# Optimization experiments

Hardware: AMD Instinct MI355X
Metric: run time of the kernel (lower is better)

## Reference

```python
import jax, jax.numpy as jnp
import numpy as np

B, HH, WW, C, HEADS = 2, 128, 128, 256, 8
D = C // HEADS


def setup_inputs() -> dict:
    key = jax.random.key(0)
    ks = jax.random.split(key, 24)
    def nrm(k, shape, s=0.02):
        return jax.random.normal(k, shape, jnp.float32) * s
    inp = {
        'x_2': jax.random.normal(ks[0], (B, HH, WW, C), jnp.float32),
        'x_4': jax.random.normal(ks[1], (B, HH, WW, C), jnp.float32),
        'x_8': jax.random.normal(ks[2], (B, HH, WW, C), jnp.float32),
        'y':   jax.random.normal(ks[3], (B, HH, WW, C), jnp.float32),
        'Wqm': nrm(ks[4], (C, C)), 'Wkm': nrm(ks[5], (C, C)), 'Wvm': nrm(ks[6], (C, C)),
        'Wk2': nrm(ks[7], (C, C)), 'Wv2': nrm(ks[8], (C, C)),
        'Wk4': nrm(ks[9], (C, C)), 'Wv4': nrm(ks[10], (C, C)),
        'Wk8': nrm(ks[11], (C, C)), 'Wv8': nrm(ks[12], (C, C)),
        'rescalem': jnp.ones((HEADS, 1, 1), jnp.float32),
        'rescale2': jnp.ones((HEADS, 1, 1), jnp.float32),
        'rescale4': jnp.ones((HEADS, 1, 1), jnp.float32),
        'rescale8': jnp.ones((HEADS, 1, 1), jnp.float32),
        'Wproj': nrm(ks[13], (C, C)), 'bproj': jnp.zeros((C,), jnp.float32),
        'Wpos1': nrm(ks[14], (C, 1, 3, 3)), 'Wpos2': nrm(ks[15], (C, 1, 3, 3)),
    }
    return inp


def _l2norm(x):
    # F.normalize(p=2, dim=-1): x / max(||x||_2, eps)
    return x / jnp.maximum(jnp.linalg.norm(x, axis=-1, keepdims=True), 1e-12)


def _heads_T(t):
    # (b, n, h*d) -> (b, h, d, n)  (split heads then transpose last two dims)
    b, n, _ = t.shape
    return t.reshape(b, n, HEADS, D).transpose(0, 2, 3, 1)


def _dwconv(x, w):
    # x: NCHW, w: (C,1,3,3) depthwise
    return jax.lax.conv_general_dilated(
        x, w, (1, 1), 'SAME',
        dimension_numbers=('NCHW', 'OIHW', 'NCHW'),
        feature_group_count=C)


def reference(x_2, x_4, x_8, y,
              Wqm, Wkm, Wvm, Wk2, Wv2, Wk4, Wv4, Wk8, Wv8,
              rescalem, rescale2, rescale4, rescale8,
              Wproj, bproj, Wpos1, Wpos2):
    b, h, w, c = y.shape
    n = h * w
    x2 = x_2.reshape(b, n, c)
    x4 = x_4.reshape(b, n, c)
    x8 = x_8.reshape(b, n, c)
    yf = y.reshape(b, n, c)

    q_inpm = yf @ Wqm.T
    v_inpm = yf @ Wvm.T
    qm = _l2norm(_heads_T(q_inpm))  # (b,heads,d,n), L2-normalized over n

    def branch(k_inp, v_inp, rescale):
        k = _l2norm(_heads_T(k_inp))   # (b,heads,d,n)
        v = _heads_T(v_inp)            # (b,heads,d,n)
        attn = jnp.einsum('bhdn,bhen->bhde', k, qm) * rescale  # (b,heads,d,d)
        attn = jax.nn.softmax(attn, axis=-1)
        return jnp.einsum('bhde,bhen->bhdn', attn, v)

    # NOTE: original code uses rescale4 for the x8 branch (faithful to source).
    xo = (branch(yf @ Wkm.T, v_inpm, rescalem)
          + branch(x2 @ Wk2.T, x2 @ Wv2.T, rescale2)
          + branch(x4 @ Wk4.T, x4 @ Wv4.T, rescale4)
          + branch(x8 @ Wk8.T, x8 @ Wv8.T, rescale4))

    # (b,heads,d,n) -> (b,n,heads*d)
    xo = xo.transpose(0, 3, 1, 2).reshape(b, n, HEADS * D)
    out_c = (xo @ Wproj.T + bproj).reshape(b, h, w, c)

    p = v_inpm.reshape(b, h, w, c).transpose(0, 3, 1, 2)  # NCHW
    p = _dwconv(p, Wpos1)
    p = jax.nn.gelu(p, approximate=False)
    p = _dwconv(p, Wpos2)
    out_p = p.transpose(0, 2, 3, 1)

    return out_c + out_p
```

## Files before the change

### kernel.cpp

```cpp
#include <hip/hip_runtime.h>
#include <hip/hip_bf16.h>
#include <math.h>

typedef short bf16x8 __attribute__((ext_vector_type(8)));
typedef float f32x4 __attribute__((ext_vector_type(4)));

#define MFMA16(a,b,c) __builtin_amdgcn_mfma_f32_16x16x32_bf16(a,b,c,0,0,0)

__device__ inline short f2bf(float f){
  union{ __hip_bfloat16 h; short s; } u;
  u.h = __float2bfloat16(f);
  return u.s;
}
__device__ inline float bf2f(short s){
  uint32_t u = ((uint32_t)(uint16_t)s) << 16;
  return __builtin_bit_cast(float, u);
}
__device__ inline void store8bf(short* dst, float4 a, float4 b){
  union{ short s[8]; int4 q; } u;
  u.s[0]=f2bf(a.x); u.s[1]=f2bf(a.y); u.s[2]=f2bf(a.z); u.s[3]=f2bf(a.w);
  u.s[4]=f2bf(b.x); u.s[5]=f2bf(b.y); u.s[6]=f2bf(b.z); u.s[7]=f2bf(b.w);
  *(int4*)dst = u.q;
}

__device__ inline void gld16(const void* g, void* l){
  __builtin_amdgcn_global_load_lds(
      (const __attribute__((address_space(1))) unsigned int*)g,
      (__attribute__((address_space(3))) unsigned int*)l, 16, 0, 0);
}

__global__ __launch_bounds__(256) void k_cvt(const float* __restrict__ src, short* __restrict__ dst, int n){
  int i = blockIdx.x*256 + threadIdx.x;
  if(i < n) dst[i] = f2bf(src[i]);
}

__global__ __launch_bounds__(256) void k_wvt(const float* __restrict__ wm, const float* __restrict__ w2,
                                             const float* __restrict__ w4, const float* __restrict__ w8,
                                             short* __restrict__ wvT){
  int t = blockIdx.x*256 + threadIdx.x;
  int br = t >> 16; int rem = t & 65535; int a = rem >> 8, j = rem & 255;
  const float* w = (br==0)? wm : (br==1)? w2 : (br==2)? w4 : w8;
  wvT[t] = f2bf(w[j*256 + a]);
}

__global__ __launch_bounds__(256) void k_wT(const float* __restrict__ w1, const float* __restrict__ w2,
                                            float* __restrict__ wT){
  int t = blockIdx.x*256 + threadIdx.x;
  if(t >= 4608) return;
  int cv = t / 2304; int rem = t % 2304; int tap = rem >> 8; int c = rem & 255;
  const float* w = cv ? w2 : w1;
  wT[t] = w[c*9 + tap];
}

__global__ __launch_bounds__(256) void k_pack(const float* __restrict__ x2, const float* __restrict__ x4,
                                              const float* __restrict__ x8, const float* __restrict__ y,
                                              short* __restrict__ xt){
  int sb = blockIdx.z; int s = sb >> 1, b = sb & 1;
  const float* src = ((s==0)? y : (s==1)? x2 : (s==2)? x4 : x8) + (size_t)b*16384*256;
  __shared__ short tile[64*264];
  int t = threadIdx.x, l = t & 63, w = t >> 6;
  int n0 = blockIdx.x*64;
  #pragma unroll
  for(int p=0;p<16;++p){
    int row = p*4 + w;
    float4 v = *(const float4*)(src + (size_t)(n0+row)*256 + 4*l);
    union{ short s4[4]; int2 q; } u;
    u.s4[0]=f2bf(v.x); u.s4[1]=f2bf(v.y); u.s4[2]=f2bf(v.z); u.s4[3]=f2bf(v.w);
    *(int2*)&tile[row*264 + 4*l] = u.q;
  }
  __syncthreads();
  int c = t;
  short* outb = xt + ((size_t)sb*512 + (n0>>5))*8192;
  #pragma unroll
  for(int ti=0; ti<2; ++ti){
    union{ short v[32]; int4 q4[4]; } rowv;
    #pragma unroll
    for(int j=0;j<32;++j) rowv.v[j] = tile[(ti*32+j)*264 + c];
    char* ob = (char*)(outb + (size_t)ti*8192 + c*32);
    #pragma unroll
    for(int hi=0;hi<4;++hi)
      *(int4*)(ob + ((hi ^ (c&3))<<4)) = rowv.q4[hi];
  }
}

__device__ inline bf16x8 tfrag(const short* base, int c, int hi){
  int byte = c*64 + ((hi ^ (c&3))<<4);
  return *(const bf16x8*)((const char*)base + byte);
}

__global__ __launch_bounds__(512,2) void k_cov(const short* __restrict__ xt, float* __restrict__ covF){
  int jb = blockIdx.x;
  int ck = blockIdx.y;
  int j = jb >> 1, b = jb & 1;
  int t = threadIdx.x, l = t & 63, w = t >> 6;
  int lr = l & 15, hi = l >> 4;
  __shared__ short lds2[2][16384];
  int su = (j < 4) ? 0 : (j - 3);
  int sv = (j == 0) ? 0 : ((j < 4) ? j : (j - 3));
  int sym = (su == sv);
  const short* Ug = xt + (size_t)(su*2+b)*512*8192;
  const short* Vg = xt + (size_t)(sv*2+b)*512*8192;
  int nt0 = ck*32;

  f32x4 acc[2][16];
  #pragma unroll
  for(int i=0;i<2;++i)
    #pragma unroll
    for(int n2=0;n2<16;++n2) acc[i][n2] = (f32x4){0.f,0.f,0.f,0.f};

  #define STAGE(bufi, kk) do{                                                   \
    const short* Ut_ = Ug + (size_t)(nt0+(kk))*8192;                            \
    short* dst_ = &lds2[bufi][0];                                               \
    if(sym){                                                                    \
      _Pragma("unroll")                                                         \
      for(int i_=0;i_<2;++i_){ int ch_ = w*2+i_;                                \
        gld16(Ut_ + ch_*512 + l*8, dst_ + ch_*512); }                           \
    } else {                                                                    \
      const short* Vt_ = Vg + (size_t)(nt0+(kk))*8192;                          \
      _Pragma("unroll")                                                         \
      for(int i_=0;i_<4;++i_){ int ch_ = w*4+i_;                                \
        const short* g_ = (ch_<16) ? (Ut_ + ch_*512 + l*8)                      \
                                   : (Vt_ + (ch_-16)*512 + l*8);                \
        gld16(g_, dst_ + ch_*512); }                                            \
    }                                                                           \
  }while(0)

  const int vofs = sym ? 0 : 8192;

  STAGE(0, 0);
  __syncthreads();
  for(int k=0;k<32;++k){
    int cur = k & 1;
    if(k < 31) STAGE(cur^1, k+1);
    const short* Ub = &lds2[cur][0];
    const short* Vb = Ub + vofs;
    bf16x8 a0 = tfrag(Ub, w*32 + lr, hi);
    bf16x8 a1 = tfrag(Ub, w*32 + 16 + lr, hi);
    #pragma unroll
    for(int nt=0;nt<16;++nt){
      bf16x8 bb = tfrag(Vb, nt*16 + lr, hi);
      acc[0][nt] = MFMA16(a0, bb, acc[0][nt]);
      acc[1][nt] = MFMA16(a1, bb, acc[1][nt]);
    }
    __syncthreads();
  }
  #undef STAGE

  float* cov = covF + (size_t)jb*65536;
  #pragma unroll
  for(int rt=0;rt<2;++rt)
    #pragma unroll
    for(int nt=0;nt<16;++nt)
      #pragma unroll
      for(int r=0;r<4;++r){
        int row = w*32 + rt*16 + 4*hi + r;
        int col = nt*16 + lr;
        atomicAdd(&cov[(size_t)row*256 + col], acc[rt][nt][r]);
      }
}

__device__ inline void mm_32x256(const short (*wA)[264], const short* __restrict__ covbf,
                                 short (*tmp)[264], int t){
  int l = t & 63, w = t >> 6;
  int mt = w >> 1, ntb = (w & 1)*8;
  f32x4 acc[8];
  #pragma unroll
  for(int i=0;i<8;++i) acc[i] = (f32x4){0.f,0.f,0.f,0.f};
  #pragma unroll
  for(int kk=0; kk<8; ++kk){
    bf16x8 a = *(const bf16x8*)&wA[16*mt + (l&15)][kk*32 + 8*(l>>4)];
    #pragma unroll
    for(int n=0; n<8; ++n){
      int j = (ntb+n)*16 + (l&15);
      bf16x8 bb = *(const bf16x8*)&covbf[(size_t)j*256 + kk*32 + 8*(l>>4)];
      acc[n] = MFMA16(a, bb, acc[n]);
    }
  }
  #pragma unroll
  for(int n=0;n<8;++n)
    #pragma unroll
    for(int r=0;r<4;++r)
      tmp[16*mt + 4*(l>>4) + r][(ntb+n)*16 + (l&15)] = f2bf(acc[n][r]);
}
__device__ inline void mm_32x32(const short (*A)[264], const short (*Bw)[264], float (*M)[33], int t){
  int l = t & 63, w = t >> 6;
  int mt = w >> 1, nt = w & 1;
  f32x4 acc = (f32x4){0.f,0.f,0.f,0.f};
  #pragma unroll
  for(int kk=0; kk<8; ++kk){
    bf16x8 a = *(const bf16x8*)&A[16*mt + (l&15)][kk*32 + 8*(l>>4)];
    bf16x8 b = *(const bf16x8*)&Bw[16*nt + (l&15)][kk*32 + 8*(l>>4)];
    acc = MFMA16(a, b, acc);
  }
  #pragma unroll
  for(int r=0;r<4;++r)
    M[16*mt + 4*(l>>4) + r][16*nt + (l&15)] = acc[r];
}

__global__ __launch_bounds__(256) void k_attn(
    const float* __restrict__ Wq, const float* __restrict__ Wkm, const float* __restrict__ Wk2,
    const float* __restrict__ Wk4, const float* __restrict__ Wk8,
    const float* __restrict__ rsm, const float* __restrict__ rs2, const float* __restrict__ rs4,
    const short* __restrict__ covB, float* __restrict__ Aout){
  int h = blockIdx.x, b = blockIdx.y, br = blockIdx.z;
  int t = threadIdx.x;
  __shared__ short wk[32][264], wq[32][264], tmp[32][264];
  __shared__ float Ml[32][33];
  __shared__ float nrm[64];
  const float* Wk = (br==0)? Wkm : (br==1)? Wk2 : (br==2)? Wk4 : Wk8;
  {
    int d = t >> 3, c0 = (t & 7)*32;
    const float* pk = Wk + (size_t)(h*32+d)*256 + c0;
    const float* pq = Wq + (size_t)(h*32+d)*256 + c0;
    #pragma unroll
    for(int i=0;i<32;i+=8){
      float4 a1 = *(const float4*)(pk+i), a2 = *(const float4*)(pk+i+4);
      store8bf(&wk[d][c0+i], a1, a2);
      float4 b1 = *(const float4*)(pq+i), b2 = *(const float4*)(pq+i+4);
      store8bf(&wq[d][c0+i], b1, b2);
    }
  }
  __syncthreads();
  const short* cxy = covB + (size_t)(br*2+b)*65536;
  const short* cxx = (br==0)? cxy : covB + (size_t)(8 + (br-1)*2 + b)*65536;
  const short* cyy = covB + (size_t)b*65536;
  mm_32x256(wk, cxx, tmp, t); __syncthreads();
  mm_32x32(tmp, wk, Ml, t);   __syncthreads();
  if(t < 32) nrm[t] = Ml[t][t];
  __syncthreads();
  mm_32x256(wq, cyy, tmp, t); __syncthreads();
  mm_32x32(tmp, wq, Ml, t);   __syncthreads();
  if(t < 32) nrm[32+t] = Ml[t][t];
  __syncthreads();
  mm_32x256(wk, cxy, tmp, t); __syncthreads();
  mm_32x32(tmp, wq, Ml, t);   __syncthreads();
  if(t < 32){
    int d = t;
    const float* rs = (br==0)? rsm : (br==1)? rs2 : rs4;
    float rsv = rs[h];
    float invk = 1.f / fmaxf(sqrtf(fmaxf(nrm[d], 0.f)), 1e-12f);
    float lg[32]; float mx = -1e30f;
    #pragma unroll
    for(int e=0;e<32;++e){
      float invq = 1.f / fmaxf(sqrtf(fmaxf(nrm[32+e], 0.f)), 1e-12f);
      float v = Ml[d][e] * invk * invq * rsv;
      lg[e] = v; mx = fmaxf(mx, v);
    }
    float sum = 0.f;
    #pragma unroll
    for(int e=0;e<32;++e){ lg[e] = expf(lg[e]-mx); sum += lg[e]; }
    float inv = 1.f/sum;
    float* Ao = Aout + ((size_t)((br*2+b)*8 + h))*1024 + d*32;
    #pragma unroll
    for(int e=0;e<32;++e) Ao[e] = lg[e]*inv;
  }
}

__global__ __launch_bounds__(256) void k_qfold(const float* __restrict__ Wproj, const float* __restrict__ Ain,
                                               const short* __restrict__ wvT, short* __restrict__ qf){
  int cg = blockIdx.x, b = blockIdx.y, br = blockIdx.z;
  int t = threadIdx.x;
  __shared__ float Al[8*1036];
  __shared__ short pl[32][264];
  const float* Ag = Ain + (size_t)((br*2+b)*8)*1024;
  for(int i=t; i<8192; i+=256){
    int hh = i >> 10, dd = (i >> 5) & 31, ee = i & 31;
    Al[hh*1036 + dd*32 + ee] = Ag[i];
  }
  __syncthreads();
  {
    int c = cg*32 + (t >> 3), h = t & 7;
    const float* wpr = Wproj + (size_t)c*256 + h*32;
    float wp[32];
    #pragma unroll
    for(int i=0;i<32;i+=4){
      float4 v = *(const float4*)(wpr+i);
      wp[i]=v.x; wp[i+1]=v.y; wp[i+2]=v.z; wp[i+3]=v.w;
    }
    float pv[32];
    #pragma unroll
    for(int e=0;e<32;++e) pv[e]=0.f;
    const float* Ah = Al + h*1036;
    #pragma unroll
    for(int d=0; d<32; ++d){
      float wpd = wp[d];
      #pragma unroll
      for(int e=0;e<32;e+=4){
        float4 av = *(const float4*)&Ah[d*32+e];
        pv[e]   += wpd*av.x; pv[e+1] += wpd*av.y;
        pv[e+2] += wpd*av.z; pv[e+3] += wpd*av.w;
      }
    }
    #pragma unroll
    for(int e=0;e<32;++e) pl[t>>3][h*32+e] = f2bf(pv[e]);
  }
  __syncthreads();
  {
    int l = t & 63, w = t >> 6, mt = w >> 1, ntb = (w & 1)*8;
    const short* wvt = wvT + (size_t)br*65536;
    f32x4 acc[8];
    #pragma unroll
    for(int i=0;i<8;++i) acc[i] = (f32x4){0.f,0.f,0.f,0.f};
    #pragma unroll
    for(int kk=0; kk<8; ++kk){
      bf16x8 a = *(const bf16x8*)&pl[16*mt + (l&15)][kk*32 + 8*(l>>4)];
      #pragma unroll
      for(int n=0;n<8;++n){
        int arow = (ntb+n)*16 + (l&15);
        bf16x8 bb = *(const bf16x8*)&wvt[(size_t)arow*256 + kk*32 + 8*(l>>4)];
        acc[n] = MFMA16(a, bb, acc[n]);
      }
    }
    short* qfp = qf + (size_t)(br*2+b)*65536;
    #pragma unroll
    for(int n=0;n<8;++n)
      #pragma unroll
      for(int r=0;r<4;++r){
        int row = cg*32 + 16*mt + 4*(l>>4) + r;
        int col = (ntb+n)*16 + (l&15);
        qfp[(size_t)row*256 + col] = f2bf(acc[n][r]);
      }
  }
}

__device__ inline void at_write4(short* base, int row, int l, float4 v){
  union{ short s[4]; int2 q; } u;
  u.s[0]=f2bf(v.x); u.s[1]=f2bf(v.y); u.s[2]=f2bf(v.z); u.s[3]=f2bf(v.w);
  int byte = row*512 + 8*l;
  byte ^= ((row&7)<<4);
  *(int2*)((char*)base + byte) = u.q;
}
__device__ inline bf16x8 at_read8(const short* base, int row, int kk, int q){
  int byte = row*512 + kk*64 + q*16;
  byte ^= ((row&7)<<4);
  return *(const bf16x8*)((const char*)base + byte);
}

__global__ __launch_bounds__(256,2) void k_vm(const float* __restrict__ y, const short* __restrict__ wB,
                                              short* __restrict__ vm){
  int t = threadIdx.x, l = t & 63, w = t >> 6;
  size_t m0 = (size_t)blockIdx.x*64;
  __shared__ short at[64*256];
  #pragma unroll
  for(int rr=0; rr<16; ++rr){
    int row = w*16 + rr;
    float4 v = *(const float4*)(y + (m0+row)*256 + 4*l);
    at_write4(at, row, l, v);
  }
  __syncthreads();
  f32x4 acc[4][4];
  #pragma unroll
  for(int i=0;i<4;++i)
    #pragma unroll
    for(int n2=0;n2<4;++n2) acc[i][n2] = (f32x4){0.f,0.f,0.f,0.f};
  #pragma unroll
  for(int kk=0; kk<8; ++kk){
    bf16x8 a[4];
    #pragma unroll
    for(int rt=0;rt<4;++rt) a[rt] = at_read8(at, rt*16 + (l&15), kk, l>>4);
    #pragma unroll
    for(int nt=0;nt<4;++nt){
      int bc = (w*4+nt)*16 + (l&15);
      bf16x8 bb = *(const bf16x8*)&wB[(size_t)bc*256 + kk*32 + 8*(l>>4)];
      #pragma unroll
      for(int rt=0;rt<4;++rt) acc[rt][nt] = MFMA16(a[rt], bb, acc[rt][nt]);
    }
  }
  #pragma unroll
  for(int rt=0;rt<4;++rt)
    #pragma unroll
    for(int nt=0;nt<4;++nt)
      #pragma unroll
      for(int r=0;r<4;++r){
        size_t row = m0 + rt*16 + 4*(l>>4) + r;
        int col = (w*4+nt)*16 + (l&15);
        vm[row*256 + col] = f2bf(acc[rt][nt][r]);
      }
}

__global__ __launch_bounds__(256) void k_conv(const short* __restrict__ in, const float* __restrict__ wT,
                                              short* __restrict__ out, int do_gelu){
  int tid = blockIdx.x*256 + threadIdx.x;
  int cg = tid & 31; int pix = tid >> 5;
  int x = pix & 127, yy = (pix >> 7) & 127, b = pix >> 14;
  int c0 = cg*8;
  float acc[8];
  #pragma unroll
  for(int i=0;i<8;++i) acc[i]=0.f;
  #pragma unroll
  for(int ky=0; ky<3; ++ky){
    int sy = yy + ky - 1;
    if(sy < 0 || sy > 127) continue;
    #pragma unroll
    for(int kx=0; kx<3; ++kx){
      int sx = x + kx - 1;
      if(sx < 0 || sx > 127) continue;
      const float* wp = wT + (ky*3+kx)*256 + c0;
      float4 w0 = *(const float4*)wp;
      float4 w1 = *(const float4*)(wp+4);
      const short* p = in + ((size_t)(((b<<7)+sy)<<7) + sx)*256 + c0;
      union{ int4 q; short s[8]; } u;
      u.q = *(const int4*)p;
      acc[0] += bf2f(u.s[0])*w0.x; acc[1] += bf2f(u.s[1])*w0.y;
      acc[2] += bf2f(u.s[2])*w0.z; acc[3] += bf2f(u.s[3])*w0.w;
      acc[4] += bf2f(u.s[4])*w1.x; acc[5] += bf2f(u.s[5])*w1.y;
      acc[6] += bf2f(u.s[6])*w1.z; acc[7] += bf2f(u.s[7])*w1.w;
    }
  }
  if(do_gelu){
    #pragma unroll
    for(int cc=0;cc<8;++cc)
      acc[cc] = 0.5f*acc[cc]*(1.f + erff(acc[cc]*0.70710678118654752f));
  }
  union{ int4 q; short s[8]; } o;
  #pragma unroll
  for(int cc=0;cc<8;++cc) o.s[cc] = f2bf(acc[cc]);
  *(int4*)(out + (size_t)pix*256 + c0) = o.q;
}

__global__ __launch_bounds__(256,2) void k_final(const float* __restrict__ y, const float* __restrict__ x2,
                                                 const float* __restrict__ x4, const float* __restrict__ x8,
                                                 const short* __restrict__ qf, const float* __restrict__ bproj,
                                                 const short* __restrict__ pos, float* __restrict__ out){
  int t = threadIdx.x, l = t & 63, w = t >> 6;
  size_t m0 = (size_t)blockIdx.x*64;
  int b = (int)(m0 >> 14);
  __shared__ short at[64*256];
  f32x4 acc[4][4];
  #pragma unroll
  for(int i=0;i<4;++i)
    #pragma unroll
    for(int n2=0;n2<4;++n2) acc[i][n2] = (f32x4){0.f,0.f,0.f,0.f};
  const float* srcs[4] = {y, x2, x4, x8};
  #pragma unroll 1
  for(int br=0; br<4; ++br){
    __syncthreads();
    #pragma unroll
    for(int rr=0; rr<16; ++rr){
      int row = w*16 + rr;
      float4 v = *(const float4*)(srcs[br] + (m0+row)*256 + 4*l);
      at_write4(at, row, l, v);
    }
    __syncthreads();
    const short* qb = qf + (size_t)(br*2+b)*65536;
    #pragma unroll
    for(int kk=0; kk<8; ++kk){
      bf16x8 a[4];
      #pragma unroll
      for(int rt=0;rt<4;++rt) a[rt] = at_read8(at, rt*16 + (l&15), kk, l>>4);
      #pragma unroll
      for(int nt=0;nt<4;++nt){
        int bc = (w*4+nt)*16 + (l&15);
        bf16x8 bb = *(const bf16x8*)&qb[(size_t)bc*256 + kk*32 + 8*(l>>4)];
        #pragma unroll
        for(int rt=0;rt<4;++rt) acc[rt][nt] = MFMA16(a[rt], bb, acc[rt][nt]);
      }
    }
  }
  #pragma unroll
  for(int rt=0;rt<4;++rt)
    #pragma unroll
    for(int nt=0;nt<4;++nt)
      #pragma unroll
      for(int r=0;r<4;++r){
        size_t row = m0 + rt*16 + 4*(l>>4) + r;
        int col = (w*4+nt)*16 + (l&15);
        out[row*256 + col] = acc[rt][nt][r] + bproj[col] + bf2f(pos[row*256 + col]);
      }
}

extern "C" void kernel_launch(void* const* d_in, const int* in_sizes, int n_in,
                              void* d_out, int out_size, void* d_ws, size_t ws_size,
                              hipStream_t stream){
  (void)in_sizes; (void)n_in; (void)out_size; (void)ws_size;
  const float* x2   = (const float*)d_in[0];
  const float* x4   = (const float*)d_in[1];
  const float* x8   = (const float*)d_in[2];
  const float* y    = (const float*)d_in[3];
  const float* Wq   = (const float*)d_in[4];
  const float* Wkm  = (const float*)d_in[5];
  const float* Wvm  = (const float*)d_in[6];
  const float* Wk2  = (const float*)d_in[7];
  const float* Wv2  = (const float*)d_in[8];
  const float* Wk4  = (const float*)d_in[9];
  const float* Wv4  = (const float*)d_in[10];
  const float* Wk8  = (const float*)d_in[11];
  const float* Wv8  = (const float*)d_in[12];
  const float* rsm  = (const float*)d_in[13];
  const float* rs2  = (const float*)d_in[14];
  const float* rs4  = (const float*)d_in[15];
  const float* Wproj= (const float*)d_in[17];
  const float* bproj= (const float*)d_in[18];
  const float* Wp1  = (const float*)d_in[19];
  const float* Wp2  = (const float*)d_in[20];
  float* out = (float*)d_out;

  char* ws = (char*)d_ws;
  short* XT2  = (short*)(ws + 0);
  short* VM   = (short*)(ws + 0);
  short* GBUF = (short*)(ws + 16777216);
  short* POS  = (short*)(ws + 33554432);
  float* wT   = (float*)(ws + 50331648);
  float* covF = (float*)(ws + 67108864);
  short* covB = (short*)(ws + 70778880);
  float* Aout = (float*)(ws + 72613888);
  short* QF   = (short*)(ws + 72876032);
  short* WvmB = (short*)(ws + 73924608);
  short* WvT  = (short*)(ws + 74055680);

  hipMemsetAsync(covF, 0, 3670016, stream);
  k_cvt  <<<256, 256, 0, stream>>>(Wvm, WvmB, 65536);
  k_wvt  <<<1024, 256, 0, stream>>>(Wvm, Wv2, Wv4, Wv8, WvT);
  k_pack <<<dim3(256,1,8), 256, 0, stream>>>(x2, x4, x8, y, XT2);
  k_cov  <<<dim3(14,16), 512, 0, stream>>>(XT2, covF);
  k_cvt  <<<3584, 256, 0, stream>>>(covF, covB, 917504);
  k_wT   <<<18, 256, 0, stream>>>(Wp1, Wp2, wT);
  k_attn <<<dim3(8,2,4), 256, 0, stream>>>(Wq, Wkm, Wk2, Wk4, Wk8, rsm, rs2, rs4, covB, Aout);
  k_qfold<<<dim3(8,2,4), 256, 0, stream>>>(Wproj, Aout, WvT, QF);
  k_vm   <<<512, 256, 0, stream>>>(y, WvmB, VM);
  k_conv <<<4096, 256, 0, stream>>>(VM, wT, GBUF, 1);
  k_conv <<<4096, 256, 0, stream>>>(GBUF, wT + 2304, POS, 0);
  k_final<<<512, 256, 0, stream>>>(y, x2, x4, x8, QF, bproj, POS, out);
}
```

Measured before the change: 287.8 us.

## Load covariance MFMA fragments directly from global memory, drop LDS staging

The covariance kernel no longer stages tiles through double-buffered LDS with global_load_lds and barriers. Each wave now reads its bf16 fragments straight from global memory, and the XOR swizzle in the pack layout is removed to match. The grid doubles along the reduction split (32 chunks of 16 tiles) to add parallelism. This removes LDS traffic and block-wide syncs, but it gives up data reuse across waves, which now read the same V tiles from cache repeatedly. It also doubles the atomicAdd traffic into the covariance buffer.

```diff
diff --git a/kernel.cpp b/kernel.cpp
--- a/kernel.cpp
+++ b/kernel.cpp
@@ -21,12 +21,6 @@
   u.s[0]=f2bf(a.x); u.s[1]=f2bf(a.y); u.s[2]=f2bf(a.z); u.s[3]=f2bf(a.w);
   u.s[4]=f2bf(b.x); u.s[5]=f2bf(b.y); u.s[6]=f2bf(b.z); u.s[7]=f2bf(b.w);
   *(int4*)dst = u.q;
-}
-
-__device__ inline void gld16(const void* g, void* l){
-  __builtin_amdgcn_global_load_lds(
-      (const __attribute__((address_space(1))) unsigned int*)g,
-      (__attribute__((address_space(3))) unsigned int*)l, 16, 0, 0);
 }
 
 __global__ __launch_bounds__(256) void k_cvt(const float* __restrict__ src, short* __restrict__ dst, int n){
@@ -79,13 +73,8 @@
     char* ob = (char*)(outb + (size_t)ti*8192 + c*32);
     #pragma unroll
     for(int hi=0;hi<4;++hi)
-      *(int4*)(ob + ((hi ^ (c&3))<<4)) = rowv.q4[hi];
-  }
-}
-
-__device__ inline bf16x8 tfrag(const short* base, int c, int hi){
-  int byte = c*64 + ((hi ^ (c&3))<<4);
-  return *(const bf16x8*)((const char*)base + byte);
+      *(int4*)(ob + (hi<<4)) = rowv.q4[hi];
+  }
 }
 
 __global__ __launch_bounds__(512,2) void k_cov(const short* __restrict__ xt, float* __restrict__ covF){
@@ -94,13 +83,10 @@
   int j = jb >> 1, b = jb & 1;
   int t = threadIdx.x, l = t & 63, w = t >> 6;
   int lr = l & 15, hi = l >> 4;
-  __shared__ short lds2[2][16384];
   int su = (j < 4) ? 0 : (j - 3);
   int sv = (j == 0) ? 0 : ((j < 4) ? j : (j - 3));
-  int sym = (su == sv);
   const short* Ug = xt + (size_t)(su*2+b)*512*8192;
   const short* Vg = xt + (size_t)(sv*2+b)*512*8192;
-  int nt0 = ck*32;
 
   f32x4 acc[2][16];
   #pragma unroll
@@ -108,43 +94,22 @@
     #pragma unroll
     for(int n2=0;n2<16;++n2) acc[i][n2] = (f32x4){0.f,0.f,0.f,0.f};
 
-  #define STAGE(bufi, kk) do{                                                   \
-    const short* Ut_ = Ug + (size_t)(nt0+(kk))*8192;                            \
-    short* dst_ = &lds2[bufi][0];                                               \
-    if(sym){                                                                    \
-      _Pragma("unroll")                                                         \
-      for(int i_=0;i_<2;++i_){ int ch_ = w*2+i_;                                \
-        gld16(Ut_ + ch_*512 + l*8, dst_ + ch_*512); }                           \
-    } else {                                                                    \
-      const short* Vt_ = Vg + (size_t)(nt0+(kk))*8192;                          \
-      _Pragma("unroll")                                                         \
-      for(int i_=0;i_<4;++i_){ int ch_ = w*4+i_;                                \
-        const short* g_ = (ch_<16) ? (Ut_ + ch_*512 + l*8)                      \
-                                   : (Vt_ + (ch_-16)*512 + l*8);                \
-        gld16(g_, dst_ + ch_*512); }                                            \
-    }                                                                           \
-  }while(0)
-
-  const int vofs = sym ? 0 : 8192;
-
-  STAGE(0, 0);
-  __syncthreads();
-  for(int k=0;k<32;++k){
-    int cur = k & 1;
-    if(k < 31) STAGE(cur^1, k+1);
-    const short* Ub = &lds2[cur][0];
-    const short* Vb = Ub + vofs;
-    bf16x8 a0 = tfrag(Ub, w*32 + lr, hi);
-    bf16x8 a1 = tfrag(Ub, w*32 + 16 + lr, hi);
+  #pragma unroll 1
+  for(int k=0;k<16;++k){
+    const short* tU = Ug + (size_t)(ck*16+k)*8192;
+    const short* tV = Vg + (size_t)(ck*16+k)*8192;
+    bf16x8 a0 = *(const bf16x8*)(tU + (w*32+lr)*32 + hi*8);
+    bf16x8 a1 = *(const bf16x8*)(tU + (w*32+16+lr)*32 + hi*8);
+    bf16x8 bv[16];
+    #pragma unroll
+    for(int nt=0;nt<16;++nt)
+      bv[nt] = *(const bf16x8*)(tV + (nt*16+lr)*32 + hi*8);
     #pragma unroll
     for(int nt=0;nt<16;++nt){
-      bf16x8 bb = tfrag(Vb, nt*16 + lr, hi);
-      acc[0][nt] = MFMA16(a0, bb, acc[0][nt]);
-      acc[1][nt] = MFMA16(a1, bb, acc[1][nt]);
-    }
-    __syncthreads();
-  }
-  #undef STAGE
+      acc[0][nt] = MFMA16(a0, bv[nt], acc[0][nt]);
+      acc[1][nt] = MFMA16(a1, bv[nt], acc[1][nt]);
+    }
+  }
 
   float* cov = covF + (size_t)jb*65536;
   #pragma unroll
@@ -512,7 +477,7 @@
   k_cvt  <<<256, 256, 0, stream>>>(Wvm, WvmB, 65536);
   k_wvt  <<<1024, 256, 0, stream>>>(Wvm, Wv2, Wv4, Wv8, WvT);
   k_pack <<<dim3(256,1,8), 256, 0, stream>>>(x2, x4, x8, y, XT2);
-  k_cov  <<<dim3(14,16), 512, 0, stream>>>(XT2, covF);
+  k_cov  <<<dim3(14,32), 512, 0, stream>>>(XT2, covF);
   k_cvt  <<<3584, 256, 0, stream>>>(covF, covB, 917504);
   k_wT   <<<18, 256, 0, stream>>>(Wp1, Wp2, wT);
   k_attn <<<dim3(8,2,4), 256, 0, stream>>>(Wq, Wkm, Wk2, Wk4, Wk8, rsm, rs2, rs4, covB, Aout);
```

Result: slower. 365.4 us (+27.0%).

## Pipeline covariance kernel loads two stages deep with explicit vmcnt waits and new swizzle

Applied to the files above, without the earlier changes.

The covariance kernel's loop now keeps two global-to-LDS stages in flight instead of one. It uses raw s_barrier calls and explicit s_waitcnt vmcnt counts in place of __syncthreads, and splits the symmetric and asymmetric paths into separate loops so the branch is no longer inside the staging macro. The LDS/transposed-layout XOR swizzle changes from (c&3) to ((c>>1)&3), which alters the bank-conflict pattern of the fragment reads. The intent is to hide global load latency behind the MFMA work and to cut LDS conflicts, at the risk of fragile manual waitcnt accounting.

```diff
diff --git a/kernel.cpp b/kernel.cpp
--- a/kernel.cpp
+++ b/kernel.cpp
@@ -28,6 +28,9 @@
       (const __attribute__((address_space(1))) unsigned int*)g,
       (__attribute__((address_space(3))) unsigned int*)l, 16, 0, 0);
 }
+
+#define BARC() do{ asm volatile("":::"memory"); __builtin_amdgcn_s_barrier(); \
+                   asm volatile("":::"memory"); }while(0)
 
 __global__ __launch_bounds__(256) void k_cvt(const float* __restrict__ src, short* __restrict__ dst, int n){
   int i = blockIdx.x*256 + threadIdx.x;
@@ -71,6 +74,7 @@
   __syncthreads();
   int c = t;
   short* outb = xt + ((size_t)sb*512 + (n0>>5))*8192;
+  int sw = (c>>1)&3;
   #pragma unroll
   for(int ti=0; ti<2; ++ti){
     union{ short v[32]; int4 q4[4]; } rowv;
@@ -79,12 +83,12 @@
     char* ob = (char*)(outb + (size_t)ti*8192 + c*32);
     #pragma unroll
     for(int hi=0;hi<4;++hi)
-      *(int4*)(ob + ((hi ^ (c&3))<<4)) = rowv.q4[hi];
+      *(int4*)(ob + ((hi ^ sw)<<4)) = rowv.q4[hi];
   }
 }
 
 __device__ inline bf16x8 tfrag(const short* base, int c, int hi){
-  int byte = c*64 + ((hi ^ (c&3))<<4);
+  int byte = c*64 + ((hi ^ ((c>>1)&3))<<4);
   return *(const bf16x8*)((const char*)base + byte);
 }
 
@@ -108,43 +112,77 @@
     #pragma unroll
     for(int n2=0;n2<16;++n2) acc[i][n2] = (f32x4){0.f,0.f,0.f,0.f};
 
-  #define STAGE(bufi, kk) do{                                                   \
+  #define STAGE_S(bufi, kk) do{                                                 \
     const short* Ut_ = Ug + (size_t)(nt0+(kk))*8192;                            \
     short* dst_ = &lds2[bufi][0];                                               \
-    if(sym){                                                                    \
-      _Pragma("unroll")                                                         \
-      for(int i_=0;i_<2;++i_){ int ch_ = w*2+i_;                                \
-        gld16(Ut_ + ch_*512 + l*8, dst_ + ch_*512); }                           \
-    } else {                                                                    \
-      const short* Vt_ = Vg + (size_t)(nt0+(kk))*8192;                          \
-      _Pragma("unroll")                                                         \
-      for(int i_=0;i_<4;++i_){ int ch_ = w*4+i_;                                \
-        const short* g_ = (ch_<16) ? (Ut_ + ch_*512 + l*8)                      \
-                                   : (Vt_ + (ch_-16)*512 + l*8);                \
-        gld16(g_, dst_ + ch_*512); }                                            \
+    _Pragma("unroll")                                                           \
+    for(int i_=0;i_<2;++i_){ int ch_ = w*2+i_;                                  \
+      gld16(Ut_ + ch_*512 + l*8, dst_ + ch_*512); }                             \
+  }while(0)
+  #define STAGE_A(bufi, kk) do{                                                 \
+    const short* Ut_ = Ug + (size_t)(nt0+(kk))*8192;                            \
+    const short* Vt_ = Vg + (size_t)(nt0+(kk))*8192;                            \
+    short* dst_ = &lds2[bufi][0];                                               \
+    _Pragma("unroll")                                                           \
+    for(int i_=0;i_<4;++i_){ int ch_ = w*4+i_;                                  \
+      const short* g_ = (ch_<16) ? (Ut_ + ch_*512 + l*8)                        \
+                                 : (Vt_ + (ch_-16)*512 + l*8);                  \
+      gld16(g_, dst_ + ch_*512); }                                              \
+  }while(0)
+
+  #define COMPUTE(cur, vofs) do{                                                \
+    const short* Ub_ = &lds2[cur][0];                                           \
+    const short* Vb_ = Ub_ + (vofs);                                            \
+    bf16x8 a0_ = tfrag(Ub_, w*32 + lr, hi);                                     \
+    bf16x8 a1_ = tfrag(Ub_, w*32 + 16 + lr, hi);                                \
+    _Pragma("unroll")                                                           \
+    for(int nt_=0;nt_<16;++nt_){                                                \
+      bf16x8 bb_ = tfrag(Vb_, nt_*16 + lr, hi);                                 \
+      acc[0][nt_] = MFMA16(a0_, bb_, acc[0][nt_]);                              \
+      acc[1][nt_] = MFMA16(a1_, bb_, acc[1][nt_]);                              \
     }                                                                           \
   }while(0)
 
-  const int vofs = sym ? 0 : 8192;
-
-  STAGE(0, 0);
-  __syncthreads();
-  for(int k=0;k<32;++k){
-    int cur = k & 1;
-    if(k < 31) STAGE(cur^1, k+1);
-    const short* Ub = &lds2[cur][0];
-    const short* Vb = Ub + vofs;
-    bf16x8 a0 = tfrag(Ub, w*32 + lr, hi);
-    bf16x8 a1 = tfrag(Ub, w*32 + 16 + lr, hi);
-    #pragma unroll
-    for(int nt=0;nt<16;++nt){
-      bf16x8 bb = tfrag(Vb, nt*16 + lr, hi);
-      acc[0][nt] = MFMA16(a0, bb, acc[0][nt]);
-      acc[1][nt] = MFMA16(a1, bb, acc[1][nt]);
-    }
-    __syncthreads();
-  }
-  #undef STAGE
+  if(sym){
+    STAGE_S(0, 0);
+    STAGE_S(1, 1);
+    asm volatile("s_waitcnt vmcnt(2)":::"memory");
+    BARC();
+    for(int k=0;k<32;++k){
+      int cur = k & 1;
+      COMPUTE(cur, 0);
+      if(k == 31) break;
+      BARC();
+      if(k+2 < 32){
+        STAGE_S(cur, k+2);
+        asm volatile("s_waitcnt vmcnt(2)":::"memory");
+      } else {
+        asm volatile("s_waitcnt vmcnt(0)":::"memory");
+      }
+      BARC();
+    }
+  } else {
+    STAGE_A(0, 0);
+    STAGE_A(1, 1);
+    asm volatile("s_waitcnt vmcnt(4)":::"memory");
+    BARC();
+    for(int k=0;k<32;++k){
+      int cur = k & 1;
+      COMPUTE(cur, 8192);
+      if(k == 31) break;
+      BARC();
+      if(k+2 < 32){
+        STAGE_A(cur, k+2);
+        asm volatile("s_waitcnt vmcnt(4)":::"memory");
+      } else {
+        asm volatile("s_waitcnt vmcnt(0)":::"memory");
+      }
+      BARC();
+    }
+  }
+  #undef STAGE_S
+  #undef STAGE_A
+  #undef COMPUTE
 
   float* cov = covF + (size_t)jb*65536;
   #pragma unroll
```

Measured after the change: 288.2 us. Within noise of the previous version (+0.1%).
